# Optimization experiments

Hardware: AMD Instinct MI355X
Metric: run time of the kernel (lower is better)

Reference implementation:

```python
import jax, jax.numpy as jnp
import numpy as np

ENTROPY_TEMPERATURE = 0.01
ENTROPY_LOSS_RATIO = 0.1
BETA = 0.25  # commitment loss weight


def setup_inputs() -> dict:
    key = jax.random.key(0)
    k1, k2 = jax.random.split(key)
    z = jax.random.normal(k1, (32, 32, 16, 16), dtype=jnp.float32)
    # VQ codebook [K, C]
    embedding = jax.random.normal(k2, (16384, 32), dtype=jnp.float32) * 0.05
    return {"z": z, "embedding": embedding}


def _entropy_loss(affinity):
    # faithful to compute_entropy_loss(loss_type='softmax', temperature=0.01)
    flat = affinity.reshape(-1, affinity.shape[-1]) / ENTROPY_TEMPERATURE  # [N, K]
    probs = jax.nn.softmax(flat, axis=-1)
    log_probs = jax.nn.log_softmax(flat + 1e-5, axis=-1)
    avg_probs = jnp.mean(probs, axis=0)  # [K]
    avg_entropy = -jnp.sum(avg_probs * jnp.log(avg_probs + 1e-5))
    sample_entropy = -jnp.mean(jnp.sum(probs * log_probs, axis=-1))
    return sample_entropy - avg_entropy


def reference(z, embedding):
    B, C, H, W = z.shape
    zf = jnp.transpose(z, (0, 2, 3, 1)).reshape(-1, C)  # [N, C]
    # squared L2 distances to every codebook entry: [N, K]
    d = (jnp.sum(zf * zf, axis=1, keepdims=True)
         + jnp.sum(embedding * embedding, axis=1)
         - 2.0 * (zf @ embedding.T))
    idx = jnp.argmin(d, axis=1)                # [N] nearest codes
    z_q = jnp.take(embedding, idx, axis=0)     # [N, C]

    commit_loss = jnp.mean((jax.lax.stop_gradient(z_q) - zf) ** 2)
    codebook_loss = jnp.mean((z_q - jax.lax.stop_gradient(zf)) ** 2)
    ent_loss = _entropy_loss(-d)
    loss = codebook_loss + BETA * commit_loss + ENTROPY_LOSS_RATIO * ent_loss

    # straight-through estimator
    z_q_st = zf + jax.lax.stop_gradient(z_q - zf)
    z_q_out = jnp.transpose(z_q_st.reshape(B, H, W, C), (0, 3, 1, 2))  # [B, C, H, W]
    return z_q_out, loss, idx
```

## Files before the change

kernel.cpp:

```cpp
#include <hip/hip_runtime.h>

#define KCODES 16384
#define CDIM   32
#define NROWS  8192
#define KSPLIT 8
#define CHUNK  (KCODES/KSPLIT)
#define WCODES (CHUNK/4)
#define NT     (WCODES/16)
#define MARGIN 4.0f

typedef _Float16 half8 __attribute__((ext_vector_type(8)));
typedef float    floatx4 __attribute__((ext_vector_type(4)));

#define WS_MSE   0
#define WS_PLP   1
#define WS_AVGP  16
#define WS_ENORM (16 + KCODES)
#define WS_ZNORM (16 + 2*KCODES)
#define WS_PART  (16 + 2*KCODES + NROWS)
#define WS_E16   (WS_PART + 4*KSPLIT*NROWS)
#define WS_Z16   (WS_E16 + KCODES*16)

#define OUT_LOSS (NROWS*CDIM)
#define OUT_IDX  (NROWS*CDIM + 1)

__global__ __launch_bounds__(256) void prep_kernel(const float* __restrict__ z,
                                                   const float* __restrict__ emb,
                                                   float* __restrict__ ws) {
  const int tid = threadIdx.x;
  if (blockIdx.x < 64) {
    int k = blockIdx.x * 256 + tid;
    const float4* p = (const float4*)(emb + (size_t)k * CDIM);
    _Float16* e16 = (_Float16*)(ws + WS_E16);
    float s = 0.f;
    half8 h[4];
#pragma unroll
    for (int i = 0; i < 8; ++i) {
      float4 v = p[i];
      s += v.x*v.x + v.y*v.y + v.z*v.z + v.w*v.w;
      h[i>>1][(i&1)*4+0] = (_Float16)v.x;
      h[i>>1][(i&1)*4+1] = (_Float16)v.y;
      h[i>>1][(i&1)*4+2] = (_Float16)v.z;
      h[i>>1][(i&1)*4+3] = (_Float16)v.w;
    }
    ws[WS_ENORM + k] = s;
    ws[WS_AVGP + k]  = 0.f;
    half8* dst = (half8*)(e16 + (size_t)k*32);
#pragma unroll
    for (int i = 0; i < 4; ++i) dst[i] = h[i];
  } else {
    int b = blockIdx.x - 64;
    int n = b*256 + tid;
    if (b == 0 && tid < 16) ws[tid] = 0.f;
    _Float16* z16 = (_Float16*)(ws + WS_Z16);
    float s = 0.f;
    half8 h[4];
#pragma unroll
    for (int c = 0; c < CDIM; ++c) {
      float v = z[(size_t)b*8192 + c*256 + tid];
      s = fmaf(v, v, s);
      h[c>>3][c&7] = (_Float16)v;
    }
    ws[WS_ZNORM + n] = s;
    half8* dst = (half8*)(z16 + (size_t)n*32);
#pragma unroll
    for (int i = 0; i < 4; ++i) dst[i] = h[i];
  }
}

__global__ __launch_bounds__(256) void gemm_pass(const float* __restrict__ ws_ro,
                                                 float* __restrict__ ws) {
  __shared__ float2 wdump[4][32];

  const int tid  = threadIdx.x;
  const int wv   = tid >> 6;
  const int lane = tid & 63;
  const int nn   = lane & 15;
  const int quad = lane >> 4;
  const int n0   = blockIdx.x * 32;
  const int kb   = blockIdx.y * CHUNK + wv * WCODES;

  const half8* z16v = (const half8*)(ws_ro + WS_Z16);
  const half8* e16v = (const half8*)(ws_ro + WS_E16);
  const float* enorm = ws_ro + WS_ENORM;
  const float* znorm = ws_ro + WS_ZNORM;
  float4* part = (float4*)(ws + WS_PART);

  half8 a0 = z16v[(size_t)(n0 + nn)*4 + quad];
  half8 a1 = z16v[(size_t)(n0 + 16 + nn)*4 + quad];

  float nzn2[8];
#pragma unroll
  for (int i = 0; i < 8; ++i)
    nzn2[i] = -0.5f * znorm[n0 + (i>>2)*16 + quad*4 + (i&3)];

  float t1l[8], t2l[8];
#pragma unroll
  for (int i = 0; i < 8; ++i) { t1l[i] = -3.0e38f; t2l[i] = -3.0e38f; }

  const int tagbase = wv*WCODES + nn;
  half8 bcur = e16v[(size_t)(kb + nn)*4 + quad];
  float en2c = 0.5f * enorm[kb + nn];

  for (int t = 0; t < NT; ++t) {
    const int tn = (t + 1 < NT) ? t + 1 : t;
    half8 bn   = e16v[(size_t)(kb + tn*16 + nn)*4 + quad];
    float en2n = 0.5f * enorm[kb + tn*16 + nn];

    floatx4 c0, c1;
#pragma unroll
    for (int i = 0; i < 4; ++i) { c0[i] = nzn2[i] - en2c; c1[i] = nzn2[i+4] - en2c; }

    floatx4 d0 = __builtin_amdgcn_mfma_f32_16x16x32_f16(a0, bcur, c0, 0, 0, 0);
    floatx4 d1 = __builtin_amdgcn_mfma_f32_16x16x32_f16(a1, bcur, c1, 0, 0, 0);

    const int tg = tagbase + 16*t;
#pragma unroll
    for (int i = 0; i < 8; ++i) {
      float lp = (i < 4) ? d0[i & 3] : d1[i & 3];
      float v  = __int_as_float((__float_as_int(lp) & 0xFFFFF000) | tg);
      t2l[i] = __builtin_amdgcn_fmed3f(v, t1l[i], t2l[i]);
      t1l[i] = fmaxf(t1l[i], v);
    }
    bcur = bn; en2c = en2n;
  }

#pragma unroll
  for (int i = 0; i < 8; ++i) {
    float v1 = t1l[i], v2 = t2l[i];
#pragma unroll
    for (int m = 1; m < 16; m <<= 1) {
      float o1 = __shfl_xor(v1, m);
      float o2 = __shfl_xor(v2, m);
      float mn = fminf(v1, o1);
      v1 = fmaxf(v1, o1);
      v2 = fmaxf(mn, fmaxf(v2, o2));
    }
    if (nn == 0) wdump[wv][(i>>2)*16 + quad*4 + (i&3)] = make_float2(v1, v2);
  }
  __syncthreads();

  if (tid < 32) {
    float v1 = -3.0e38f, v2 = -3.0e38f;
#pragma unroll
    for (int w = 0; w < 4; ++w) {
      float2 p = wdump[w][tid];
      float mn = fminf(v1, p.x);
      v1 = fmaxf(v1, p.x);
      v2 = fmaxf(mn, fmaxf(v2, p.y));
    }
    int b1 = __float_as_int(v1), b2 = __float_as_int(v2);
    int c1i = blockIdx.y*CHUNK + (b1 & 0xFFF);
    int c2i = blockIdx.y*CHUNK + (b2 & 0xFFF);
    float l1 = 200.f * __int_as_float(b1 & 0xFFFFF000);
    float l2 = 200.f * __int_as_float(b2 & 0xFFFFF000);
    part[(size_t)blockIdx.y*NROWS + n0 + tid] =
        make_float4(l1, __int_as_float(c1i), l2, __int_as_float(c2i));
  }
}

__global__ __launch_bounds__(64) void combine_kernel(const float* __restrict__ z,
                                                     const float* __restrict__ emb,
                                                     float* __restrict__ ws,
                                                     float* __restrict__ out) {
  const float4* part = (const float4*)(ws + WS_PART);
  int n = blockIdx.x*64 + threadIdx.x;

  float l[16]; int c[16];
#pragma unroll
  for (int ch = 0; ch < KSPLIT; ++ch) {
    float4 v = part[(size_t)ch*NROWS + n];
    l[ch*2+0] = v.x; c[ch*2+0] = __float_as_int(v.y);
    l[ch*2+1] = v.z; c[ch*2+1] = __float_as_int(v.w);
  }
  float mm = l[0];
#pragma unroll
  for (int i = 1; i < 16; ++i) mm = fmaxf(mm, l[i]);

  int bb = n >> 8, hw = n & 255;
  float zr[32];
  float zn = 0.f;
#pragma unroll
  for (int cc = 0; cc < CDIM; ++cc) {
    zr[cc] = z[(size_t)bb*8192 + cc*256 + hw];
    zn = fmaf(zr[cc], zr[cc], zn);
  }
  float bd = 3.0e38f; int bc = 0x7fffffff;
#pragma unroll
  for (int i = 0; i < 16; ++i) {
    if (l[i] > mm - MARGIN) {
      int code = c[i];
      const float4* er4 = (const float4*)(emb + (size_t)code*CDIM);
      float dot = 0.f;
#pragma unroll
      for (int q = 0; q < 8; ++q) {
        float4 e4 = er4[q];
        dot = fmaf(zr[q*4+0], e4.x, dot);
        dot = fmaf(zr[q*4+1], e4.y, dot);
        dot = fmaf(zr[q*4+2], e4.z, dot);
        dot = fmaf(zr[q*4+3], e4.w, dot);
      }
      float d = (zn + ws[WS_ENORM + code]) - 2.f*dot;
      if (d < bd || (d == bd && code < bc)) { bd = d; bc = code; }
    }
  }
  out[OUT_IDX + n] = (float)bc;

  const float* er = emb + (size_t)bc*CDIM;
  float msel = 0.f;
#pragma unroll
  for (int cc = 0; cc < CDIM; ++cc) {
    float zq = er[cc];
    float df = zq - zr[cc];
    msel = fmaf(df, df, msel);
    out[(size_t)bb*8192 + cc*256 + hw] = zr[cc] + (zq - zr[cc]);
  }
  for (int off = 1; off < 64; off <<= 1) msel += __shfl_xor(msel, off);
  if (threadIdx.x == 0) atomicAdd(&ws[WS_MSE], msel);

  float s = 0.f;
#pragma unroll
  for (int i = 0; i < 16; ++i) s += __expf(l[i] - mm);
  float lse = mm + __logf(s);

  float plp = 0.f;
#pragma unroll
  for (int i = 0; i < 16; ++i) {
    float u = l[i] - lse;
    float p = __expf(u);
    plp = fmaf(p, u, plp);
    if (p > 1e-12f) atomicAdd(&ws[WS_AVGP + c[i]], p);
  }
  for (int off = 1; off < 64; off <<= 1) plp += __shfl_xor(plp, off);
  if (threadIdx.x == 0) atomicAdd(&ws[WS_PLP], plp);
}

__global__ __launch_bounds__(256) void finalize_kernel(const float* __restrict__ ws,
                                                       float* __restrict__ out) {
  __shared__ float red[256];
  float h = 0.f;
  for (int k = threadIdx.x; k < KCODES; k += 256) {
    float ap = ws[WS_AVGP + k] * (1.f/8192.f);
    h += ap * __logf(ap + 1e-5f);
  }
  red[threadIdx.x] = h;
  __syncthreads();
  for (int st = 128; st > 0; st >>= 1) {
    if (threadIdx.x < st) red[threadIdx.x] += red[threadIdx.x + st];
    __syncthreads();
  }
  if (threadIdx.x == 0) {
    float mse        = ws[WS_MSE] * (1.f/(8192.f*32.f));
    float sample_ent = -ws[WS_PLP] * (1.f/8192.f);
    out[OUT_LOSS] = 1.25f*mse + 0.1f*(sample_ent + red[0]);
  }
}

extern "C" void kernel_launch(void* const* d_in, const int* in_sizes, int n_in,
                              void* d_out, int out_size, void* d_ws, size_t ws_size,
                              hipStream_t stream) {
  (void)in_sizes; (void)n_in; (void)out_size; (void)ws_size;
  const float* z   = (const float*)d_in[0];
  const float* emb = (const float*)d_in[1];
  float* out = (float*)d_out;
  float* ws  = (float*)d_ws;

  prep_kernel    <<<96, 256, 0, stream>>>(z, emb, ws);
  gemm_pass      <<<dim3(NROWS/32, KSPLIT), 256, 0, stream>>>(ws, ws);
  combine_kernel <<<NROWS/64, 64, 0, stream>>>(z, emb, ws, out);
  finalize_kernel<<<1, 256, 0, stream>>>(ws, out);
}
```

Before: 131.9 us.

## Fuse combine and finalize into GEMM pass via last-block atomic counters

Merges the combine and finalize kernels into the GEMM kernel. The last block to finish each row group, detected with an atomic counter, does the candidate rescoring and the loss accumulation, and a global counter picks the single block that runs the final entropy reduction. The MFMA loop is also software-pipelined one step deeper: loads run two tiles ahead and the top-2 update runs one tile behind the MFMA. The tag field shrinks to 11 bits, leaving more mantissa for the distance, and the rescoring margin is widened. This removes two kernel launches but adds serialized tail work in single blocks, and only 32 of 256 threads do the combine work.

```diff
diff --git a/kernel.cpp b/kernel.cpp
--- a/kernel.cpp
+++ b/kernel.cpp
@@ -7,22 +7,27 @@
 #define CHUNK  (KCODES/KSPLIT)
 #define WCODES (CHUNK/4)
 #define NT     (WCODES/16)
-#define MARGIN 4.0f
+#define NRG    (NROWS/32)
+#define MARGIN 6.0f
 
 typedef _Float16 half8 __attribute__((ext_vector_type(8)));
 typedef float    floatx4 __attribute__((ext_vector_type(4)));
 
 #define WS_MSE   0
 #define WS_PLP   1
+#define WS_GCNT  2
 #define WS_AVGP  16
 #define WS_ENORM (16 + KCODES)
 #define WS_ZNORM (16 + 2*KCODES)
 #define WS_PART  (16 + 2*KCODES + NROWS)
-#define WS_E16   (WS_PART + 4*KSPLIT*NROWS)
+#define WS_CNT   (WS_PART + 4*KSPLIT*NROWS)
+#define WS_E16   (WS_CNT + 256)
 #define WS_Z16   (WS_E16 + KCODES*16)
 
 #define OUT_LOSS (NROWS*CDIM)
 #define OUT_IDX  (NROWS*CDIM + 1)
+
+#define AGLOAD(p) __hip_atomic_load((p), __ATOMIC_RELAXED, __HIP_MEMORY_SCOPE_AGENT)
 
 __global__ __launch_bounds__(256) void prep_kernel(const float* __restrict__ z,
                                                    const float* __restrict__ emb,
@@ -51,7 +56,10 @@
   } else {
     int b = blockIdx.x - 64;
     int n = b*256 + tid;
-    if (b == 0 && tid < 16) ws[tid] = 0.f;
+    if (b == 0) {
+      ((int*)ws)[WS_CNT + tid] = 0;
+      if (tid < 16) ws[tid] = 0.f;
+    }
     _Float16* z16 = (_Float16*)(ws + WS_Z16);
     float s = 0.f;
     half8 h[4];
@@ -68,9 +76,13 @@
   }
 }
 
-__global__ __launch_bounds__(256) void gemm_pass(const float* __restrict__ ws_ro,
-                                                 float* __restrict__ ws) {
+__global__ __launch_bounds__(256) void gemm_pass(const float* __restrict__ z,
+                                                 const float* __restrict__ emb,
+                                                 float* __restrict__ ws,
+                                                 float* __restrict__ out) {
   __shared__ float2 wdump[4][32];
+  __shared__ float  red[256];
+  __shared__ int    flag_s;
 
   const int tid  = threadIdx.x;
   const int wv   = tid >> 6;
@@ -80,10 +92,9 @@
   const int n0   = blockIdx.x * 32;
   const int kb   = blockIdx.y * CHUNK + wv * WCODES;
 
-  const half8* z16v = (const half8*)(ws_ro + WS_Z16);
-  const half8* e16v = (const half8*)(ws_ro + WS_E16);
-  const float* enorm = ws_ro + WS_ENORM;
-  const float* znorm = ws_ro + WS_ZNORM;
+  const half8* z16v  = (const half8*)(ws + WS_Z16);
+  const float* enorm = ws + WS_ENORM;
+  const float* znorm = ws + WS_ZNORM;
   float4* part = (float4*)(ws + WS_PART);
 
   half8 a0 = z16v[(size_t)(n0 + nn)*4 + quad];
@@ -98,31 +109,55 @@
 #pragma unroll
   for (int i = 0; i < 8; ++i) { t1l[i] = -3.0e38f; t2l[i] = -3.0e38f; }
 
-  const int tagbase = wv*WCODES + nn;
-  half8 bcur = e16v[(size_t)(kb + nn)*4 + quad];
-  float en2c = 0.5f * enorm[kb + nn];
-
-  for (int t = 0; t < NT; ++t) {
-    const int tn = (t + 1 < NT) ? t + 1 : t;
-    half8 bn   = e16v[(size_t)(kb + tn*16 + nn)*4 + quad];
-    float en2n = 0.5f * enorm[kb + tn*16 + nn];
-
+  const half8* pb = (const half8*)(ws + WS_E16) + (size_t)(kb + nn)*4 + quad;
+  const float* pe = enorm + kb + nn;
+  const int tagb = wv*WCODES + nn;
+
+  half8 bB = pb[0];   float eB = pe[0];
+  half8 bC = pb[64];  float eC = pe[16];
+  floatx4 dp0, dp1;
+  {
+    float eh = 0.5f * eB;
     floatx4 c0, c1;
 #pragma unroll
-    for (int i = 0; i < 4; ++i) { c0[i] = nzn2[i] - en2c; c1[i] = nzn2[i+4] - en2c; }
-
-    floatx4 d0 = __builtin_amdgcn_mfma_f32_16x16x32_f16(a0, bcur, c0, 0, 0, 0);
-    floatx4 d1 = __builtin_amdgcn_mfma_f32_16x16x32_f16(a1, bcur, c1, 0, 0, 0);
-
-    const int tg = tagbase + 16*t;
+    for (int i = 0; i < 4; ++i) { c0[i] = nzn2[i] - eh; c1[i] = nzn2[i+4] - eh; }
+    dp0 = __builtin_amdgcn_mfma_f32_16x16x32_f16(a0, bB, c0, 0, 0, 0);
+    dp1 = __builtin_amdgcn_mfma_f32_16x16x32_f16(a1, bB, c1, 0, 0, 0);
+  }
+  bB = bC; eB = eC;
+  bC = pb[128]; eC = pe[32];
+
+  for (int t = 1; t < NT; ++t) {
+    const int tp = (t + 2 < NT) ? t + 2 : NT - 1;
+    half8 bN = pb[(size_t)64*tp];
+    float eN = pe[16*tp];
+
+    float eh = 0.5f * eB;
+    floatx4 c0, c1;
+#pragma unroll
+    for (int i = 0; i < 4; ++i) { c0[i] = nzn2[i] - eh; c1[i] = nzn2[i+4] - eh; }
+    floatx4 dn0 = __builtin_amdgcn_mfma_f32_16x16x32_f16(a0, bB, c0, 0, 0, 0);
+    floatx4 dn1 = __builtin_amdgcn_mfma_f32_16x16x32_f16(a1, bB, c1, 0, 0, 0);
+
+    const int tg = tagb + 16*(t-1);
 #pragma unroll
     for (int i = 0; i < 8; ++i) {
-      float lp = (i < 4) ? d0[i & 3] : d1[i & 3];
-      float v  = __int_as_float((__float_as_int(lp) & 0xFFFFF000) | tg);
+      float lp = (i < 4) ? dp0[i & 3] : dp1[i & 3];
+      float v  = __int_as_float((__float_as_int(lp) & 0xFFFFF800) | tg);
       t2l[i] = __builtin_amdgcn_fmed3f(v, t1l[i], t2l[i]);
       t1l[i] = fmaxf(t1l[i], v);
     }
-    bcur = bn; en2c = en2n;
+    dp0 = dn0; dp1 = dn1; bB = bC; eB = eC; bC = bN; eC = eN;
+  }
+  {
+    const int tg = tagb + 16*(NT-1);
+#pragma unroll
+    for (int i = 0; i < 8; ++i) {
+      float lp = (i < 4) ? dp0[i & 3] : dp1[i & 3];
+      float v  = __int_as_float((__float_as_int(lp) & 0xFFFFF800) | tg);
+      t2l[i] = __builtin_amdgcn_fmed3f(v, t1l[i], t2l[i]);
+      t1l[i] = fmaxf(t1l[i], v);
+    }
   }
 
 #pragma unroll
@@ -150,108 +185,115 @@
       v2 = fmaxf(mn, fmaxf(v2, p.y));
     }
     int b1 = __float_as_int(v1), b2 = __float_as_int(v2);
-    int c1i = blockIdx.y*CHUNK + (b1 & 0xFFF);
-    int c2i = blockIdx.y*CHUNK + (b2 & 0xFFF);
-    float l1 = 200.f * __int_as_float(b1 & 0xFFFFF000);
-    float l2 = 200.f * __int_as_float(b2 & 0xFFFFF000);
+    int c1i = blockIdx.y*CHUNK + (b1 & 0x7FF);
+    int c2i = blockIdx.y*CHUNK + (b2 & 0x7FF);
+    float l1 = 200.f * __int_as_float(b1 & 0xFFFFF800);
+    float l2 = 200.f * __int_as_float(b2 & 0xFFFFF800);
     part[(size_t)blockIdx.y*NROWS + n0 + tid] =
         make_float4(l1, __int_as_float(c1i), l2, __int_as_float(c2i));
   }
-}
-
-__global__ __launch_bounds__(64) void combine_kernel(const float* __restrict__ z,
-                                                     const float* __restrict__ emb,
-                                                     float* __restrict__ ws,
-                                                     float* __restrict__ out) {
-  const float4* part = (const float4*)(ws + WS_PART);
-  int n = blockIdx.x*64 + threadIdx.x;
-
-  float l[16]; int c[16];
-#pragma unroll
-  for (int ch = 0; ch < KSPLIT; ++ch) {
-    float4 v = part[(size_t)ch*NROWS + n];
-    l[ch*2+0] = v.x; c[ch*2+0] = __float_as_int(v.y);
-    l[ch*2+1] = v.z; c[ch*2+1] = __float_as_int(v.w);
-  }
-  float mm = l[0];
-#pragma unroll
-  for (int i = 1; i < 16; ++i) mm = fmaxf(mm, l[i]);
-
-  int bb = n >> 8, hw = n & 255;
-  float zr[32];
-  float zn = 0.f;
-#pragma unroll
-  for (int cc = 0; cc < CDIM; ++cc) {
-    zr[cc] = z[(size_t)bb*8192 + cc*256 + hw];
-    zn = fmaf(zr[cc], zr[cc], zn);
-  }
-  float bd = 3.0e38f; int bc = 0x7fffffff;
-#pragma unroll
-  for (int i = 0; i < 16; ++i) {
-    if (l[i] > mm - MARGIN) {
-      int code = c[i];
-      const float4* er4 = (const float4*)(emb + (size_t)code*CDIM);
-      float dot = 0.f;
-#pragma unroll
-      for (int q = 0; q < 8; ++q) {
-        float4 e4 = er4[q];
-        dot = fmaf(zr[q*4+0], e4.x, dot);
-        dot = fmaf(zr[q*4+1], e4.y, dot);
-        dot = fmaf(zr[q*4+2], e4.z, dot);
-        dot = fmaf(zr[q*4+3], e4.w, dot);
+
+  __threadfence();
+  __syncthreads();
+  if (tid == 0)
+    flag_s = (atomicAdd((int*)ws + WS_CNT + blockIdx.x, 1) == KSPLIT - 1);
+  __syncthreads();
+  if (!flag_s) return;
+  __threadfence();
+
+  if (tid < 32) {
+    int n = n0 + tid;
+    float l[16]; int c[16];
+#pragma unroll
+    for (int ch = 0; ch < KSPLIT; ++ch) {
+      const float* pp = (const float*)&part[(size_t)ch*NROWS + n];
+      l[ch*2+0] = AGLOAD(pp+0); c[ch*2+0] = __float_as_int(AGLOAD(pp+1));
+      l[ch*2+1] = AGLOAD(pp+2); c[ch*2+1] = __float_as_int(AGLOAD(pp+3));
+    }
+    float mm = l[0];
+#pragma unroll
+    for (int i = 1; i < 16; ++i) mm = fmaxf(mm, l[i]);
+
+    int bb = n >> 8, hw = n & 255;
+    float zr[32], zn = 0.f;
+#pragma unroll
+    for (int cc = 0; cc < CDIM; ++cc) {
+      zr[cc] = z[(size_t)bb*8192 + cc*256 + hw];
+      zn = fmaf(zr[cc], zr[cc], zn);
+    }
+    float bd = 3.0e38f; int bc = 0x7fffffff;
+#pragma unroll
+    for (int i = 0; i < 16; ++i) {
+      if (l[i] > mm - MARGIN) {
+        int code = c[i];
+        const float4* er4 = (const float4*)(emb + (size_t)code*CDIM);
+        float dot = 0.f;
+#pragma unroll
+        for (int q = 0; q < 8; ++q) {
+          float4 e4 = er4[q];
+          dot = fmaf(zr[q*4+0], e4.x, dot);
+          dot = fmaf(zr[q*4+1], e4.y, dot);
+          dot = fmaf(zr[q*4+2], e4.z, dot);
+          dot = fmaf(zr[q*4+3], e4.w, dot);
+        }
+        float d = (zn + enorm[code]) - 2.f*dot;
+        if (d < bd || (d == bd && code < bc)) { bd = d; bc = code; }
       }
-      float d = (zn + ws[WS_ENORM + code]) - 2.f*dot;
-      if (d < bd || (d == bd && code < bc)) { bd = d; bc = code; }
-    }
-  }
-  out[OUT_IDX + n] = (float)bc;
-
-  const float* er = emb + (size_t)bc*CDIM;
-  float msel = 0.f;
-#pragma unroll
-  for (int cc = 0; cc < CDIM; ++cc) {
-    float zq = er[cc];
-    float df = zq - zr[cc];
-    msel = fmaf(df, df, msel);
-    out[(size_t)bb*8192 + cc*256 + hw] = zr[cc] + (zq - zr[cc]);
-  }
-  for (int off = 1; off < 64; off <<= 1) msel += __shfl_xor(msel, off);
-  if (threadIdx.x == 0) atomicAdd(&ws[WS_MSE], msel);
-
-  float s = 0.f;
-#pragma unroll
-  for (int i = 0; i < 16; ++i) s += __expf(l[i] - mm);
-  float lse = mm + __logf(s);
-
-  float plp = 0.f;
-#pragma unroll
-  for (int i = 0; i < 16; ++i) {
-    float u = l[i] - lse;
-    float p = __expf(u);
-    plp = fmaf(p, u, plp);
-    if (p > 1e-12f) atomicAdd(&ws[WS_AVGP + c[i]], p);
-  }
-  for (int off = 1; off < 64; off <<= 1) plp += __shfl_xor(plp, off);
-  if (threadIdx.x == 0) atomicAdd(&ws[WS_PLP], plp);
-}
-
-__global__ __launch_bounds__(256) void finalize_kernel(const float* __restrict__ ws,
-                                                       float* __restrict__ out) {
-  __shared__ float red[256];
+    }
+    out[OUT_IDX + n] = (float)bc;
+
+    const float* er = emb + (size_t)bc*CDIM;
+    float msel = 0.f;
+#pragma unroll
+    for (int cc = 0; cc < CDIM; ++cc) {
+      float zq = er[cc];
+      float df = zq - zr[cc];
+      msel = fmaf(df, df, msel);
+      out[(size_t)bb*8192 + cc*256 + hw] = zr[cc] + (zq - zr[cc]);
+    }
+
+    float s = 0.f;
+#pragma unroll
+    for (int i = 0; i < 16; ++i) s += __expf(l[i] - mm);
+    float lse = mm + __logf(s);
+    float plp = 0.f;
+#pragma unroll
+    for (int i = 0; i < 16; ++i) {
+      float u = l[i] - lse;
+      float p = __expf(u);
+      plp = fmaf(p, u, plp);
+      if (p > 1e-12f) atomicAdd(&ws[WS_AVGP + c[i]], p);
+    }
+#pragma unroll
+    for (int off = 1; off < 32; off <<= 1) {
+      msel += __shfl_xor(msel, off);
+      plp  += __shfl_xor(plp, off);
+    }
+    if (tid == 0) { atomicAdd(&ws[WS_MSE], msel); atomicAdd(&ws[WS_PLP], plp); }
+  }
+
+  __threadfence();
+  __syncthreads();
+  if (tid == 0)
+    flag_s = (atomicAdd((int*)ws + WS_GCNT, 1) == NRG - 1);
+  __syncthreads();
+  if (!flag_s) return;
+  __threadfence();
+
   float h = 0.f;
-  for (int k = threadIdx.x; k < KCODES; k += 256) {
-    float ap = ws[WS_AVGP + k] * (1.f/8192.f);
+  for (int k = tid; k < KCODES; k += 256) {
+    float ap = AGLOAD(&ws[WS_AVGP + k]) * (1.f/8192.f);
     h += ap * __logf(ap + 1e-5f);
   }
-  red[threadIdx.x] = h;
+  red[tid] = h;
   __syncthreads();
   for (int st = 128; st > 0; st >>= 1) {
-    if (threadIdx.x < st) red[threadIdx.x] += red[threadIdx.x + st];
+    if (tid < st) red[tid] += red[tid + st];
     __syncthreads();
   }
-  if (threadIdx.x == 0) {
-    float mse        = ws[WS_MSE] * (1.f/(8192.f*32.f));
-    float sample_ent = -ws[WS_PLP] * (1.f/8192.f);
+  if (tid == 0) {
+    float mse        = AGLOAD(&ws[WS_MSE]) * (1.f/(8192.f*32.f));
+    float sample_ent = -AGLOAD(&ws[WS_PLP]) * (1.f/8192.f);
     out[OUT_LOSS] = 1.25f*mse + 0.1f*(sample_ent + red[0]);
   }
 }
@@ -265,8 +307,6 @@
   float* out = (float*)d_out;
   float* ws  = (float*)d_ws;
 
-  prep_kernel    <<<96, 256, 0, stream>>>(z, emb, ws);
-  gemm_pass      <<<dim3(NROWS/32, KSPLIT), 256, 0, stream>>>(ws, ws);
-  combine_kernel <<<NROWS/64, 64, 0, stream>>>(z, emb, ws, out);
-  finalize_kernel<<<1, 256, 0, stream>>>(ws, out);
+  prep_kernel<<<96, 256, 0, stream>>>(z, emb, ws);
+  gemm_pass  <<<dim3(NRG, KSPLIT), 256, 0, stream>>>(z, emb, ws, out);
 }
```

Measured after the change: 282.3 us. +114.0%, slower.
